# Kernel tuning notes

Measured on AMD Instinct MI355X. Metric: run time of the kernel, lower is better.

## Reference

```python
import jax, jax.numpy as jnp
import numpy as np

HIDDEN = 2880
N_HEADS = 64
N_KV_HEADS = 8
HEAD_DIM = 64
ROPE_THETA = 150000.0


def _rope(x, position_ids):
    # x: [B, H, S, D]; rotate-half RoPE as in the flax module
    inv_freq = 1.0 / (ROPE_THETA ** (jnp.arange(0, HEAD_DIM, 2, dtype=jnp.float32) / HEAD_DIM))
    b, h, s, d = x.shape
    freqs = jnp.outer(position_ids.reshape(-1).astype(jnp.float32), inv_freq)  # [B*S, D/2]
    cos = jnp.cos(freqs).reshape(b, 1, s, d // 2)
    sin = jnp.sin(freqs).reshape(b, 1, s, d // 2)
    x1, x2 = jnp.split(x, 2, axis=-1)
    return jnp.concatenate([x1 * cos - x2 * sin, x1 * sin + x2 * cos], axis=-1)


def setup_inputs() -> dict:
    key = jax.random.key(0)
    ks = jax.random.split(key, 5)
    B, S = 2, 1024
    x = jax.random.normal(ks[0], (B, S, HIDDEN), dtype=jnp.float32)
    wq = jax.random.normal(ks[1], (HIDDEN, N_HEADS * HEAD_DIM), dtype=jnp.float32) * 0.02
    wk = jax.random.normal(ks[2], (HIDDEN, N_KV_HEADS * HEAD_DIM), dtype=jnp.float32) * 0.02
    wv = jax.random.normal(ks[3], (HIDDEN, N_KV_HEADS * HEAD_DIM), dtype=jnp.float32) * 0.02
    wo = jax.random.normal(ks[4], (N_HEADS * HEAD_DIM, HIDDEN), dtype=jnp.float32) * 0.02
    position_ids = jnp.broadcast_to(jnp.arange(S, dtype=jnp.int32)[None, :], (B, S))
    return {"x": x, "wq": wq, "wk": wk, "wv": wv, "wo": wo, "position_ids": position_ids}


def reference(x, wq, wk, wv, wo, position_ids):
    b, s, _ = x.shape
    scale = 1.0 / np.sqrt(HEAD_DIM)
    q = (x @ wq).reshape(b, s, N_HEADS, HEAD_DIM).transpose(0, 2, 1, 3)       # [B,H,S,D]
    k = (x @ wk).reshape(b, s, N_KV_HEADS, HEAD_DIM).transpose(0, 2, 1, 3)    # [B,Hkv,S,D]
    v = (x @ wv).reshape(b, s, N_KV_HEADS, HEAD_DIM).transpose(0, 2, 1, 3)
    q = _rope(q, position_ids)
    k = _rope(k, position_ids)
    rep = N_HEADS // N_KV_HEADS
    k = jnp.repeat(k, rep, axis=1)  # GQA head-repeat as in original
    v = jnp.repeat(v, rep, axis=1)
    scores = jnp.einsum('bhqd,bhkd->bhqk', q, k) * scale
    causal = jnp.tril(jnp.ones((s, s), dtype=bool))[None, None, :, :]
    scores = jnp.where(causal, scores, -jnp.inf)
    probs = jax.nn.softmax(scores, axis=-1)
    out = jnp.einsum('bhqk,bhkd->bhqd', probs, v)
    out = out.transpose(0, 2, 1, 3).reshape(b, s, N_HEADS * HEAD_DIM)
    return out @ wo
```

## Files before the change

### kernel.cpp

```cpp
#include <hip/hip_runtime.h>

#define BB 2
#define SS 1024
#define HIDDEN 2880
#define NH 64
#define NKV 8
#define HD 64
#define M_TOK 2048
#define NQ 4096
#define NKVD 512
#define NQKV 5120
#define NOUT 2880
#define NOUT_PAD 2944

typedef __attribute__((ext_vector_type(8))) short short8;
typedef __attribute__((ext_vector_type(4))) float f32x4;

__device__ __forceinline__ unsigned short f2b(float x) {
  union { float f; unsigned u; } v; v.f = x;
  unsigned r = (v.u + 0x7FFFu + ((v.u >> 16) & 1u)) >> 16;
  return (unsigned short)r;
}

__device__ __forceinline__ void gload16(const void* g, void* l) {
  __builtin_amdgcn_global_load_lds(
      (const __attribute__((address_space(1))) void*)g,
      (__attribute__((address_space(3))) void*)l, 16, 0, 0);
}

__global__ __launch_bounds__(256) void cast_x_kernel(const float* __restrict__ in,
                                                     unsigned short* __restrict__ out,
                                                     int n4) {
  int idx = blockIdx.x * 256 + threadIdx.x;
  if (idx >= n4) return;
  float4 v = ((const float4*)in)[idx];
  ushort4 o;
  o.x = f2b(v.x); o.y = f2b(v.y); o.z = f2b(v.z); o.w = f2b(v.w);
  ((ushort4*)out)[idx] = o;
}

__global__ __launch_bounds__(256) void transpose_cast(const float* __restrict__ in,
                                                      long ldin,
                                                      unsigned short* __restrict__ out,
                                                      int K, int N) {
  __shared__ float t[32][33];
  const int n0 = blockIdx.x * 32, k0 = blockIdx.y * 32;
  const int tx = threadIdx.x, ty = threadIdx.y;
#pragma unroll
  for (int i = 0; i < 4; ++i) {
    int k = k0 + ty + i * 8;
    int n = n0 + tx;
    t[ty + i * 8][tx] = (n < N) ? in[(long)k * ldin + n] : 0.f;
  }
  __syncthreads();
#pragma unroll
  for (int i = 0; i < 4; ++i) {
    int n = n0 + ty + i * 8;
    int k = k0 + tx;
    out[(long)n * K + k] = f2b(t[tx][ty + i * 8]);
  }
}

__global__ __launch_bounds__(256) void rope_table(const int* __restrict__ pos,
                                                  float* __restrict__ ct,
                                                  float* __restrict__ st) {
  int tid = blockIdx.x * 256 + threadIdx.x;
  int t = tid >> 5, i = tid & 31;
  float p = (float)pos[t];
  float f = p * expf(-(float)i * (11.918390573078392f / 32.f));
  ct[tid] = cosf(f);
  st[tid] = sinf(f);
}

#define GEMM128_BODY(Aptr, Bptr, lda, NXT)                                                \
  __shared__ char lA[128 * 128];                                                          \
  __shared__ char lB[128 * 128];                                                          \
  const int tid = threadIdx.x;                                                            \
  const int lane = tid & 63;                                                              \
  const int w = tid >> 6;                                                                 \
  const int m16 = lane & 15, g4 = lane >> 4;                                              \
  const int wr = w >> 1, wc = w & 1;                                                      \
  const int _nwg = (NXT) * gridDim.y;                                                     \
  const int _hw = blockIdx.y * (NXT) + blockIdx.x;                                        \
  const int _lg = (_hw & 7) * (_nwg >> 3) + (_hw >> 3);                                   \
  const int bm = (_lg / (NXT)) * 128, bn = (_lg % (NXT)) * 128;                           \
  const size_t strb = (size_t)(lda) * 2;                                                  \
  const int srow = tid >> 3;                                                              \
  const int scolb = ((tid & 7) * 16) ^ ((srow & 7) << 4);                                 \
  const int sdst = w * 1024;                                                              \
  const char* ga0 = (const char*)(Aptr) + (size_t)(bm + srow) * strb + scolb;             \
  const char* gb0 = (const char*)(Bptr) + (size_t)(bn + srow) * strb + scolb;             \
  const int swz = (m16 & 7) << 4;                                                         \
  const int kc0 = (g4 * 16) ^ swz;                                                        \
  const int kc1 = (64 + g4 * 16) ^ swz;                                                   \
  f32x4 acc[4][4];                                                                        \
  _Pragma("unroll") for (int i = 0; i < 4; ++i)                                           \
  _Pragma("unroll") for (int j = 0; j < 4; ++j) acc[i][j] = (f32x4){0.f, 0.f, 0.f, 0.f};  \
  const int NT = (lda) >> 6;                                                              \
  for (int t = 0; t < NT; ++t) {                                                          \
    const size_t ko = (size_t)t * 128;                                                    \
    __syncthreads();                                                                      \
    _Pragma("unroll") for (int i = 0; i < 4; ++i) {                                       \
      gload16(ga0 + (size_t)(i * 32) * strb + ko, lA + i * 4096 + sdst);                  \
      gload16(gb0 + (size_t)(i * 32) * strb + ko, lB + i * 4096 + sdst);                  \
    }                                                                                     \
    __syncthreads();                                                                      \
    short8 af[4][2], bf[4][2];                                                            \
    _Pragma("unroll") for (int mq = 0; mq < 4; ++mq) {                                    \
      const int row = wr * 64 + mq * 16 + m16;                                            \
      af[mq][0] = *(const short8*)(lA + row * 128 + kc0);                                 \
      af[mq][1] = *(const short8*)(lA + row * 128 + kc1);                                 \
    }                                                                                     \
    _Pragma("unroll") for (int nf = 0; nf < 4; ++nf) {                                    \
      const int row = wc * 64 + nf * 16 + m16;                                            \
      bf[nf][0] = *(const short8*)(lB + row * 128 + kc0);                                 \
      bf[nf][1] = *(const short8*)(lB + row * 128 + kc1);                                 \
    }                                                                                     \
    __builtin_amdgcn_s_setprio(1);                                                        \
    _Pragma("unroll") for (int mq = 0; mq < 4; ++mq)                                      \
    _Pragma("unroll") for (int nf = 0; nf < 4; ++nf) {                                    \
      acc[mq][nf] = __builtin_amdgcn_mfma_f32_16x16x32_bf16(af[mq][0], bf[nf][0], acc[mq][nf], 0, 0, 0); \
      acc[mq][nf] = __builtin_amdgcn_mfma_f32_16x16x32_bf16(af[mq][1], bf[nf][1], acc[mq][nf], 0, 0, 0); \
    }                                                                                     \
    __builtin_amdgcn_s_setprio(0);                                                        \
  }

__global__ __launch_bounds__(256, 3) void gemm128(const unsigned short* __restrict__ A,
                                                  const unsigned short* __restrict__ Bt,
                                                  float* __restrict__ C,
                                                  int lda, int ldc, int Nvalid) {
  GEMM128_BODY(A, Bt, lda, 23)
#pragma unroll
  for (int mq = 0; mq < 4; ++mq) {
    const size_t row = bm + wr * 64 + mq * 16 + g4 * 4;
#pragma unroll
    for (int nf = 0; nf < 4; ++nf) {
      const int col = bn + wc * 64 + nf * 16 + m16;
      if (col < Nvalid) {
#pragma unroll
        for (int r = 0; r < 4; ++r)
          C[(row + r) * (size_t)ldc + col] = acc[mq][nf][r];
      }
    }
  }
}

__global__ __launch_bounds__(256, 3) void gemm128_qkv(const unsigned short* __restrict__ A,
                                                      const unsigned short* __restrict__ Bt,
                                                      const float* __restrict__ ct,
                                                      const float* __restrict__ st,
                                                      unsigned short* __restrict__ qb,
                                                      unsigned short* __restrict__ kb,
                                                      unsigned short* __restrict__ vtb,
                                                      int lda) {
  GEMM128_BODY(A, Bt, lda, 40)
  const int region = (bn < 4096) ? 0 : ((bn < 4608) ? 1 : 2);
#pragma unroll
  for (int mq = 0; mq < 4; ++mq) {
    const int row = bm + wr * 64 + mq * 16 + g4 * 4;
    if (region == 2) {
#pragma unroll
      for (int nf = 0; nf < 4; ++nf) {
        const int d = (bn - 4608) + wc * 64 + nf * 16 + m16;
#pragma unroll
        for (int r = 0; r < 4; ++r) {
          const int t = row + r;
          const int b = t >> 10, sidx = t & 1023;
          vtb[((size_t)(b * NKVD + d)) * SS + sidx] = f2b(acc[mq][nf][r]);
        }
      }
    } else {
#pragma unroll
      for (int nf = 0; nf < 2; ++nf) {
        const int i = nf * 16 + m16;
#pragma unroll
        for (int r = 0; r < 4; ++r) {
          const int t = row + r;
          const int b = t >> 10, sidx = t & 1023;
          const float x1 = acc[mq][nf][r], x2 = acc[mq][nf + 2][r];
          const float c = ct[t * 32 + i], s = st[t * 32 + i];
          if (region == 0) {
            const int h = (bn >> 6) + wc;
            unsigned short* dst = qb + (((size_t)(b * NH + h)) * SS + sidx) * HD;
            dst[i]      = f2b((x1 * c - x2 * s) * 0.125f);
            dst[i + 32] = f2b((x1 * s + x2 * c) * 0.125f);
          } else {
            const int hk = ((bn - 4096) >> 6) + wc;
            unsigned short* dst = kb + (((size_t)(b * NKV + hk)) * SS + sidx) * HD;
            dst[i]      = f2b(x1 * c - x2 * s);
            dst[i + 32] = f2b(x1 * s + x2 * c);
          }
        }
      }
    }
  }
}

__global__ __launch_bounds__(512) void attn_fwd(const unsigned short* __restrict__ qb,
                                                const unsigned short* __restrict__ kb,
                                                const unsigned short* __restrict__ vtb,
                                                unsigned short* __restrict__ ao) {
  __shared__ unsigned short kB[2][64 * 64];
  __shared__ unsigned short vB[2][64 * 64];
  __shared__ unsigned short pB[8][32 * 64];
  const int tid = threadIdx.x, lane = tid & 63, w = tid >> 6;
  const int lid = blockIdx.y * 4 + blockIdx.x;
  const int j = lid & 255, half = lid >> 8;
  const int qblk = half ? ((j & 1) ? 2 : 3) : ((j & 1) ? 1 : 0);
  const int bh = j >> 1;
  const int b = bh >> 6, h = bh & 63, hkv = h >> 3;
  const int m16 = lane & 15, g4 = lane >> 4;
  const int rbase = qblk * 256 + w * 32;

  const unsigned short* qp =
      qb + (((size_t)(b * NH + h)) * SS + rbase + m16) * HD + g4 * 8;
  const short8 q00 = *(const short8*)(qp);
  const short8 q01 = *(const short8*)(qp + 32);
  const short8 q10 = *(const short8*)(qp + 16 * HD);
  const short8 q11 = *(const short8*)(qp + 16 * HD + 32);

  const char* kbp = (const char*)(kb + ((size_t)(b * NKV + hkv)) * SS * HD);
  const char* vbp = (const char*)(vtb + ((size_t)(b * NKV + hkv)) * HD * SS);

  const int lrow = lane >> 3;
  const int lcolb = ((lane & 7) * 16) ^ ((lrow & 7) << 4);
  unsigned short* kDst0 = &kB[0][w * 512];
  unsigned short* kDst1 = &kB[1][w * 512];
  unsigned short* vDst0 = &vB[0][w * 512];
  unsigned short* vDst1 = &vB[1][w * 512];
  const size_t kRowOff = (size_t)(w * 8 + lrow) * 128 + lcolb;
  const size_t vRowOff = (size_t)(w * 8 + lrow) * 2048 + lcolb;

  const short8 ones = {(short)0x3F80, (short)0x3F80, (short)0x3F80, (short)0x3F80,
                       (short)0x3F80, (short)0x3F80, (short)0x3F80, (short)0x3F80};

  f32x4 o0[4], o1[4];
#pragma unroll
  for (int n = 0; n < 4; ++n) { o0[n] = (f32x4){0,0,0,0}; o1[n] = (f32x4){0,0,0,0}; }
  f32x4 lacc0 = (f32x4){0,0,0,0}, lacc1 = (f32x4){0,0,0,0};
  float mrow0[4] = {-1e30f,-1e30f,-1e30f,-1e30f};
  float mrow1[4] = {-1e30f,-1e30f,-1e30f,-1e30f};

  char* pw = (char*)pB[w];
  const int swz_m = (m16 & 7) << 4;
  const int nt = (qblk + 1) * 4;

  gload16(kbp + kRowOff, kDst0);
  gload16(vbp + vRowOff, vDst0);
  __syncthreads();

  for (int t = 0; t < nt; ++t) {
    const int k0 = t * 64;
    const char* kLds = (const char*)kB[t & 1];
    const char* vLds = (const char*)vB[t & 1];
    if (t + 1 < nt) {
      if (t & 1) { gload16(kbp + (size_t)(t + 1) * 8192 + kRowOff, kDst0);
                   gload16(vbp + (size_t)(t + 1) * 128  + vRowOff, vDst0); }
      else       { gload16(kbp + (size_t)(t + 1) * 8192 + kRowOff, kDst1);
                   gload16(vbp + (size_t)(t + 1) * 128  + vRowOff, vDst1); }
    }
    if (k0 < rbase + 32) {
      short8 kf0[4], kf1[4];
#pragma unroll
      for (int kf = 0; kf < 4; ++kf) {
        const int rb = (kf * 16 + m16) * 128;
        kf0[kf] = *(const short8*)(kLds + ((rb + g4 * 16) ^ swz_m));
        kf1[kf] = *(const short8*)(kLds + ((rb + 64 + g4 * 16) ^ swz_m));
      }
      f32x4 s0[4], s1[4];
      __builtin_amdgcn_s_setprio(1);
#pragma unroll
      for (int kf = 0; kf < 4; ++kf) {
        f32x4 z = (f32x4){0,0,0,0};
        z = __builtin_amdgcn_mfma_f32_16x16x32_bf16(q00, kf0[kf], z, 0, 0, 0);
        z = __builtin_amdgcn_mfma_f32_16x16x32_bf16(q01, kf1[kf], z, 0, 0, 0);
        s0[kf] = z;
        f32x4 z2 = (f32x4){0,0,0,0};
        z2 = __builtin_amdgcn_mfma_f32_16x16x32_bf16(q10, kf0[kf], z2, 0, 0, 0);
        z2 = __builtin_amdgcn_mfma_f32_16x16x32_bf16(q11, kf1[kf], z2, 0, 0, 0);
        s1[kf] = z2;
      }
      __builtin_amdgcn_s_setprio(0);
      if (k0 + 63 >= rbase) {
#pragma unroll
        for (int kf = 0; kf < 4; ++kf)
#pragma unroll
          for (int r = 0; r < 4; ++r) {
            const int col = k0 + kf * 16 + m16;
            if (col > rbase + g4 * 4 + r)      s0[kf][r] = -1e30f;
            if (col > rbase + 16 + g4 * 4 + r) s1[kf][r] = -1e30f;
          }
      }
      int grow = 0;
#pragma unroll
      for (int kf = 0; kf < 4; ++kf)
#pragma unroll
        for (int r = 0; r < 4; ++r) {
          grow |= (s0[kf][r] > mrow0[r] + 8.f);
          grow |= (s1[kf][r] > mrow1[r] + 8.f);
        }
      if (__any(grow)) {
        float mx0[4], mx1[4];
#pragma unroll
        for (int r = 0; r < 4; ++r) {
          mx0[r] = fmaxf(fmaxf(s0[0][r], s0[1][r]), fmaxf(s0[2][r], s0[3][r]));
          mx1[r] = fmaxf(fmaxf(s1[0][r], s1[1][r]), fmaxf(s1[2][r], s1[3][r]));
        }
#pragma unroll
        for (int off = 1; off <= 8; off <<= 1)
#pragma unroll
          for (int r = 0; r < 4; ++r) {
            mx0[r] = fmaxf(mx0[r], __shfl_xor(mx0[r], off));
            mx1[r] = fmaxf(mx1[r], __shfl_xor(mx1[r], off));
          }
#pragma unroll
        for (int r = 0; r < 4; ++r) {
          float mn0 = fmaxf(mrow0[r], mx0[r]);
          float sc0 = __expf(mrow0[r] - mn0);
          mrow0[r] = mn0; lacc0[r] *= sc0;
          float mn1 = fmaxf(mrow1[r], mx1[r]);
          float sc1 = __expf(mrow1[r] - mn1);
          mrow1[r] = mn1; lacc1[r] *= sc1;
#pragma unroll
          for (int n = 0; n < 4; ++n) { o0[n][r] *= sc0; o1[n][r] *= sc1; }
        }
      }
#pragma unroll
      for (int kf = 0; kf < 4; ++kf)
#pragma unroll
        for (int r = 0; r < 4; ++r) {
          const int colb = (kf * 16 + m16) * 2;
          int row = g4 * 4 + r;
          *(unsigned short*)(pw + ((row * 128 + colb) ^ ((row & 7) << 4))) =
              f2b(__expf(s0[kf][r] - mrow0[r]));
          row += 16;
          *(unsigned short*)(pw + ((row * 128 + colb) ^ ((row & 7) << 4))) =
              f2b(__expf(s1[kf][r] - mrow1[r]));
        }
      const int prb0 = m16 * 128, prb1 = (16 + m16) * 128;
      short8 pf00 = *(const short8*)(pw + ((prb0 + g4 * 16) ^ swz_m));
      short8 pf01 = *(const short8*)(pw + ((prb0 + 64 + g4 * 16) ^ swz_m));
      short8 pf10 = *(const short8*)(pw + ((prb1 + g4 * 16) ^ swz_m));
      short8 pf11 = *(const short8*)(pw + ((prb1 + 64 + g4 * 16) ^ swz_m));
      __builtin_amdgcn_s_setprio(1);
      lacc0 = __builtin_amdgcn_mfma_f32_16x16x32_bf16(pf00, ones, lacc0, 0, 0, 0);
      lacc0 = __builtin_amdgcn_mfma_f32_16x16x32_bf16(pf01, ones, lacc0, 0, 0, 0);
      lacc1 = __builtin_amdgcn_mfma_f32_16x16x32_bf16(pf10, ones, lacc1, 0, 0, 0);
      lacc1 = __builtin_amdgcn_mfma_f32_16x16x32_bf16(pf11, ones, lacc1, 0, 0, 0);
#pragma unroll
      for (int n = 0; n < 4; ++n) {
        const int rb = (n * 16 + m16) * 128;
        short8 vf0 = *(const short8*)(vLds + ((rb + g4 * 16) ^ swz_m));
        short8 vf1 = *(const short8*)(vLds + ((rb + 64 + g4 * 16) ^ swz_m));
        o0[n] = __builtin_amdgcn_mfma_f32_16x16x32_bf16(pf00, vf0, o0[n], 0, 0, 0);
        o0[n] = __builtin_amdgcn_mfma_f32_16x16x32_bf16(pf01, vf1, o0[n], 0, 0, 0);
        o1[n] = __builtin_amdgcn_mfma_f32_16x16x32_bf16(pf10, vf0, o1[n], 0, 0, 0);
        o1[n] = __builtin_amdgcn_mfma_f32_16x16x32_bf16(pf11, vf1, o1[n], 0, 0, 0);
      }
      __builtin_amdgcn_s_setprio(0);
    }
    __syncthreads();
  }

  float inv0[4], inv1[4];
#pragma unroll
  for (int r = 0; r < 4; ++r) { inv0[r] = 1.f / lacc0[r]; inv1[r] = 1.f / lacc1[r]; }
  const size_t row0 = (size_t)b * SS + rbase + g4 * 4;
#pragma unroll
  for (int n = 0; n < 4; ++n)
#pragma unroll
    for (int r = 0; r < 4; ++r) {
      ao[(row0 + r) * (size_t)NQ + h * 64 + n * 16 + m16] = f2b(o0[n][r] * inv0[r]);
      ao[(row0 + 16 + r) * (size_t)NQ + h * 64 + n * 16 + m16] = f2b(o1[n][r] * inv1[r]);
    }
}

constexpr size_t OFF_XB    = 0;
constexpr size_t OFF_WQKVT = 11796480;
constexpr size_t OFF_WOT   = 41287680;
constexpr size_t OFF_COS   = 65404928;
constexpr size_t OFF_SIN   = 65667072;
constexpr size_t OFF_QB    = 65929216;
constexpr size_t OFF_KB    = 82706432;
constexpr size_t OFF_VTB   = 84803584;
constexpr size_t OFF_ATTNB = 86900736;

extern "C" void kernel_launch(void* const* d_in, const int* in_sizes, int n_in,
                              void* d_out, int out_size, void* d_ws, size_t ws_size,
                              hipStream_t stream) {
  const float* x  = (const float*)d_in[0];
  const float* wq = (const float*)d_in[1];
  const float* wk = (const float*)d_in[2];
  const float* wv = (const float*)d_in[3];
  const float* wo = (const float*)d_in[4];
  const int* pos  = (const int*)d_in[5];
  float* out = (float*)d_out;
  char* ws = (char*)d_ws;

  unsigned short* xb    = (unsigned short*)(ws + OFF_XB);
  unsigned short* wqkvt = (unsigned short*)(ws + OFF_WQKVT);
  unsigned short* wot   = (unsigned short*)(ws + OFF_WOT);
  float* ct             = (float*)(ws + OFF_COS);
  float* st             = (float*)(ws + OFF_SIN);
  unsigned short* qbuf  = (unsigned short*)(ws + OFF_QB);
  unsigned short* kbuf  = (unsigned short*)(ws + OFF_KB);
  unsigned short* vtb   = (unsigned short*)(ws + OFF_VTB);
  unsigned short* attnb = (unsigned short*)(ws + OFF_ATTNB);

  cast_x_kernel<<<(M_TOK * HIDDEN / 4 + 255) / 256, 256, 0, stream>>>(x, xb, M_TOK * HIDDEN / 4);
  rope_table<<<(M_TOK * 32) / 256, 256, 0, stream>>>(pos, ct, st);
  transpose_cast<<<dim3(NQ / 32, HIDDEN / 32), dim3(32, 8), 0, stream>>>(
      wq, NQ, wqkvt, HIDDEN, NQ);
  transpose_cast<<<dim3(NKVD / 32, HIDDEN / 32), dim3(32, 8), 0, stream>>>(
      wk, NKVD, wqkvt + (size_t)NQ * HIDDEN, HIDDEN, NKVD);
  transpose_cast<<<dim3(NKVD / 32, HIDDEN / 32), dim3(32, 8), 0, stream>>>(
      wv, NKVD, wqkvt + (size_t)(NQ + NKVD) * HIDDEN, HIDDEN, NKVD);
  transpose_cast<<<dim3(NOUT_PAD / 32, NQ / 32), dim3(32, 8), 0, stream>>>(
      wo, NOUT, wot, NQ, NOUT);
  gemm128_qkv<<<dim3(NQKV / 128, M_TOK / 128), 256, 0, stream>>>(
      xb, wqkvt, ct, st, qbuf, kbuf, vtb, HIDDEN);
  attn_fwd<<<dim3(4, BB * NH), 512, 0, stream>>>(qbuf, kbuf, vtb, attnb);
  gemm128<<<dim3(NOUT_PAD / 128, M_TOK / 128), 256, 0, stream>>>(
      attnb, wot, out, NQ, NOUT, NOUT);
}
```

Before: 233.0 us.

## Double-buffer LDS tiles in output projection GEMM to overlap loads with MFMA

```diff
diff --git a/kernel.cpp b/kernel.cpp
--- a/kernel.cpp
+++ b/kernel.cpp
@@ -27,6 +27,9 @@
       (const __attribute__((address_space(1))) void*)g,
       (__attribute__((address_space(3))) void*)l, 16, 0, 0);
 }
+
+#define BARR() asm volatile("s_barrier" ::: "memory")
+#define VMC0() asm volatile("s_waitcnt vmcnt(0)" ::: "memory")
 
 __global__ __launch_bounds__(256) void cast_x_kernel(const float* __restrict__ in,
                                                      unsigned short* __restrict__ out,
@@ -125,11 +128,81 @@
     __builtin_amdgcn_s_setprio(0);                                                        \
   }
 
-__global__ __launch_bounds__(256, 3) void gemm128(const unsigned short* __restrict__ A,
-                                                  const unsigned short* __restrict__ Bt,
-                                                  float* __restrict__ C,
-                                                  int lda, int ldc, int Nvalid) {
-  GEMM128_BODY(A, Bt, lda, 23)
+__global__ __launch_bounds__(256, 2) void gemm128_db(const unsigned short* __restrict__ A,
+                                                     const unsigned short* __restrict__ Bt,
+                                                     float* __restrict__ C,
+                                                     int lda, int ldc, int Nvalid) {
+  __shared__ char lA[2][128 * 128];
+  __shared__ char lB[2][128 * 128];
+  const int tid = threadIdx.x;
+  const int lane = tid & 63;
+  const int w = tid >> 6;
+  const int m16 = lane & 15, g4 = lane >> 4;
+  const int wr = w >> 1, wc = w & 1;
+  const int NXT = 23;
+  const int _nwg = NXT * gridDim.y;
+  const int _hw = blockIdx.y * NXT + blockIdx.x;
+  const int _lg = (_hw & 7) * (_nwg >> 3) + (_hw >> 3);
+  const int bm = (_lg / NXT) * 128, bn = (_lg % NXT) * 128;
+  const size_t strb = (size_t)lda * 2;
+  const int srow = tid >> 3;
+  const int scolb = ((tid & 7) * 16) ^ ((srow & 7) << 4);
+  const int sdst = w * 1024;
+  const char* ga0 = (const char*)A + (size_t)(bm + srow) * strb + scolb;
+  const char* gb0 = (const char*)Bt + (size_t)(bn + srow) * strb + scolb;
+  const int swz = (m16 & 7) << 4;
+  const int kc0 = (g4 * 16) ^ swz;
+  const int kc1 = (64 + g4 * 16) ^ swz;
+
+  auto stage = [&](int buf, int t) {
+    const size_t ko = (size_t)t * 128;
+#pragma unroll
+    for (int i = 0; i < 4; ++i) {
+      gload16(ga0 + (size_t)(i * 32) * strb + ko, lA[buf] + i * 4096 + sdst);
+      gload16(gb0 + (size_t)(i * 32) * strb + ko, lB[buf] + i * 4096 + sdst);
+    }
+  };
+
+  f32x4 acc[4][4];
+#pragma unroll
+  for (int i = 0; i < 4; ++i)
+#pragma unroll
+    for (int j = 0; j < 4; ++j) acc[i][j] = (f32x4){0.f, 0.f, 0.f, 0.f};
+
+  const int NT = lda >> 6;
+  stage(0, 0);
+  VMC0();
+  BARR();
+
+  for (int t = 0; t < NT; ++t) {
+    const int cur = t & 1;
+    if (t + 1 < NT) stage(cur ^ 1, t + 1);
+    short8 af[4][2], bf[4][2];
+#pragma unroll
+    for (int mq = 0; mq < 4; ++mq) {
+      const int row = wr * 64 + mq * 16 + m16;
+      af[mq][0] = *(const short8*)(lA[cur] + row * 128 + kc0);
+      af[mq][1] = *(const short8*)(lA[cur] + row * 128 + kc1);
+    }
+#pragma unroll
+    for (int nf = 0; nf < 4; ++nf) {
+      const int row = wc * 64 + nf * 16 + m16;
+      bf[nf][0] = *(const short8*)(lB[cur] + row * 128 + kc0);
+      bf[nf][1] = *(const short8*)(lB[cur] + row * 128 + kc1);
+    }
+    __builtin_amdgcn_s_setprio(1);
+#pragma unroll
+    for (int mq = 0; mq < 4; ++mq)
+#pragma unroll
+      for (int nf = 0; nf < 4; ++nf) {
+        acc[mq][nf] = __builtin_amdgcn_mfma_f32_16x16x32_bf16(af[mq][0], bf[nf][0], acc[mq][nf], 0, 0, 0);
+        acc[mq][nf] = __builtin_amdgcn_mfma_f32_16x16x32_bf16(af[mq][1], bf[nf][1], acc[mq][nf], 0, 0, 0);
+      }
+    __builtin_amdgcn_s_setprio(0);
+    VMC0();
+    BARR();
+  }
+
 #pragma unroll
   for (int mq = 0; mq < 4; ++mq) {
     const size_t row = bm + wr * 64 + mq * 16 + g4 * 4;
@@ -420,6 +493,6 @@
   gemm128_qkv<<<dim3(NQKV / 128, M_TOK / 128), 256, 0, stream>>>(
       xb, wqkvt, ct, st, qbuf, kbuf, vtb, HIDDEN);
   attn_fwd<<<dim3(4, BB * NH), 512, 0, stream>>>(qbuf, kbuf, vtb, attnb);
-  gemm128<<<dim3(NOUT_PAD / 128, M_TOK / 128), 256, 0, stream>>>(
+  gemm128_db<<<dim3(NOUT_PAD / 128, M_TOK / 128), 256, 0, stream>>>(
       attnb, wot, out, NQ, NOUT, NOUT);
 }
```

Result: no change. 236.0 us (+1.3%).
